# Kernel tuning notes

Hardware: AMD Instinct MI355X
Metric: run time of the kernel (lower is better)

The kernel has to match this reference:

```python
import jax, jax.numpy as jnp
import numpy as np

N_NODES = 40000
N_EDGES = 640000
IN_CH = 128
HID = 32
HEADS = 4
OUT_CH = 112
NEG_SLOPE = 0.2  # PyG GATConv default LeakyReLU slope


def _gat_conv(x, src, dst, W, a_src, a_dst, bias, heads, ch, concat):
    # x: [N, F_in], W: [F_in, heads*ch], a_src/a_dst: [heads, ch], bias: [heads*ch] or [ch]
    N = x.shape[0]
    h = (x @ W).reshape(N, heads, ch)                       # [N, H, C]
    al_src = jnp.sum(h * a_src, axis=-1)                    # [N, H]
    al_dst = jnp.sum(h * a_dst, axis=-1)                    # [N, H]
    e = jax.nn.leaky_relu(al_src[src] + al_dst[dst], NEG_SLOPE)  # [E, H]
    # numerically stable segment softmax over incoming edges of each dst node
    m = jax.ops.segment_max(e, dst, num_segments=N)
    m = jnp.where(jnp.isfinite(m), m, 0.0)
    ex = jnp.exp(e - m[dst])
    den = jax.ops.segment_sum(ex, dst, num_segments=N)
    alpha = ex / (den[dst] + 1e-16)                         # [E, H]
    out = jax.ops.segment_sum(h[src] * alpha[:, :, None], dst, num_segments=N)  # [N, H, C]
    out = out.reshape(N, heads * ch) if concat else out.mean(axis=1)
    return out + bias


def setup_inputs() -> dict:
    key = jax.random.key(0)
    ks = jax.random.split(key, 10)
    x = jax.random.normal(ks[0], (N_NODES, IN_CH), dtype=jnp.float32)
    edge_index = jax.random.randint(ks[1], (2, N_EDGES), 0, N_NODES, dtype=jnp.int64)
    s1 = 1.0 / np.sqrt(IN_CH)
    s2 = 1.0 / np.sqrt(HID * HEADS)
    s3 = 1.0 / np.sqrt(HID)
    return {
        "x": x,
        "edge_index": edge_index,
        "W1": jax.random.normal(ks[2], (IN_CH, HEADS * HID), dtype=jnp.float32) * s1,
        "a_src1": jax.random.normal(ks[3], (HEADS, HID), dtype=jnp.float32) * s3,
        "a_dst1": jax.random.normal(ks[4], (HEADS, HID), dtype=jnp.float32) * s3,
        "b1": jnp.zeros((HEADS * HID,), dtype=jnp.float32),
        "W2": jax.random.normal(ks[5], (HEADS * HID, HID), dtype=jnp.float32) * s2,
        "a_src2": jax.random.normal(ks[6], (1, HID), dtype=jnp.float32) * s3,
        "a_dst2": jax.random.normal(ks[7], (1, HID), dtype=jnp.float32) * s3,
        "b2": jnp.zeros((HID,), dtype=jnp.float32),
        "W_out": jax.random.normal(ks[8], (HID, OUT_CH), dtype=jnp.float32) * s3,
        "b_out": jnp.zeros((OUT_CH,), dtype=jnp.float32),
    }


def reference(x, edge_index, W1, a_src1, a_dst1, b1, W2, a_src2, a_dst2, b2, W_out, b_out):
    N = x.shape[0]
    # PyG GATConv adds self-loops by default
    loops = jnp.arange(N, dtype=edge_index.dtype)
    src = jnp.concatenate([edge_index[0], loops])
    dst = jnp.concatenate([edge_index[1], loops])
    h = _gat_conv(x, src, dst, W1, a_src1, a_dst1, b1, HEADS, HID, concat=True)
    h = jax.nn.elu(h)  # dropout is identity in eval mode
    h = _gat_conv(h, src, dst, W2, a_src2, a_dst2, b2, 1, HID, concat=True)
    h = jax.nn.elu(h)
    return h @ W_out + b_out
```

## Files before the change

### kernel.cpp

```cpp
#include <hip/hip_runtime.h>

#define N_NODES 40000
#define E_EDGES 640000
#define E_TOT   (E_EDGES + N_NODES)
#define SCAN_BLOCKS ((N_NODES + 255) / 256)
#define G1_BLOCKS 625
#define HIST_BLOCKS ((E_EDGES + 255) / 256)

typedef unsigned int uint;
typedef unsigned short ushort;
typedef __attribute__((ext_vector_type(8))) short short8v;
typedef __attribute__((ext_vector_type(4))) float f32x4;

__device__ __forceinline__ ushort f2bf(float f) {
    uint u = __float_as_uint(f);
    u += 0x7FFFu + ((u >> 16) & 1u);
    return (ushort)(u >> 16);
}
__device__ __forceinline__ uint pk_bf(float lo, float hi) {
    return (uint)f2bf(lo) | ((uint)f2bf(hi) << 16);
}
__device__ __forceinline__ float bf_lo(uint w) { return __uint_as_float(w << 16); }
__device__ __forceinline__ float bf_hi(uint w) { return __uint_as_float(w & 0xFFFF0000u); }
__device__ __forceinline__ float bf2f(ushort v) { return __uint_as_float((uint)v << 16); }

__global__ __launch_bounds__(256) void prep_kernel(
    const float* __restrict__ W1, int4* __restrict__ cnt4, ushort* __restrict__ Wf)
{
    if (blockIdx.x < 40) {
        const int i = blockIdx.x * 256 + threadIdx.x;
        if (i < 40064 / 4) cnt4[i] = make_int4(1, 1, 1, 1);
        return;
    }
    const int s = (blockIdx.x - 40) * 256 + threadIdx.x;
    if (s >= 2048) return;
    const int kk = s >> 9;
    const int rem = s & 511;
    const int ct = rem >> 6;
    const int l = rem & 63;
    const int k0 = kk * 32 + (l >> 4) * 8;
    const int col = ct * 16 + (l & 15);
    uint4 o;
    o.x = pk_bf(W1[(k0 + 0) * 128 + col], W1[(k0 + 1) * 128 + col]);
    o.y = pk_bf(W1[(k0 + 2) * 128 + col], W1[(k0 + 3) * 128 + col]);
    o.z = pk_bf(W1[(k0 + 4) * 128 + col], W1[(k0 + 5) * 128 + col]);
    o.w = pk_bf(W1[(k0 + 6) * 128 + col], W1[(k0 + 7) * 128 + col]);
    ((uint4*)Wf)[s] = o;
}

__global__ __launch_bounds__(256) void gemm1_hist_kernel(
    const float* __restrict__ x, const ushort* __restrict__ Wf,
    const float* __restrict__ a_src, const float* __restrict__ a_dst,
    ushort* __restrict__ h1b, float* __restrict__ asrc, float* __restrict__ adst,
    const int* __restrict__ eidx, int* __restrict__ cnt, int* __restrict__ rank)
{
    if (blockIdx.x >= G1_BLOCKS) {
        const int e = (blockIdx.x - G1_BLOCKS) * 256 + threadIdx.x;
        if (e < E_EDGES)
            rank[e] = atomicAdd(&cnt[eidx[E_EDGES + e]], 1);
        return;
    }

    const int wv = threadIdx.x >> 6;
    const int lane = threadIdx.x & 63;
    const int rowbase = blockIdx.x * 64 + wv * 16;
    const int arow = rowbase + (lane & 15);
    const int kof = (lane >> 4) * 8;

    f32x4 acc0 = {0.f,0.f,0.f,0.f}, acc1 = {0.f,0.f,0.f,0.f};
    f32x4 acc2 = {0.f,0.f,0.f,0.f}, acc3 = {0.f,0.f,0.f,0.f};
    f32x4 acc4 = {0.f,0.f,0.f,0.f}, acc5 = {0.f,0.f,0.f,0.f};
    f32x4 acc6 = {0.f,0.f,0.f,0.f}, acc7 = {0.f,0.f,0.f,0.f};

    const short8v* WfV = (const short8v*)Wf;
#pragma unroll
    for (int kk = 0; kk < 4; ++kk) {
        const float* ap = &x[(size_t)arow * 128 + kk * 32 + kof];
        const float4 a0 = *(const float4*)ap;
        const float4 a1 = *(const float4*)(ap + 4);
        short8v af;
        af[0] = (short)f2bf(a0.x); af[1] = (short)f2bf(a0.y);
        af[2] = (short)f2bf(a0.z); af[3] = (short)f2bf(a0.w);
        af[4] = (short)f2bf(a1.x); af[5] = (short)f2bf(a1.y);
        af[6] = (short)f2bf(a1.z); af[7] = (short)f2bf(a1.w);
        const int base = kk * 8 * 64 + lane;
        acc0 = __builtin_amdgcn_mfma_f32_16x16x32_bf16(af, WfV[base + 0 * 64], acc0, 0, 0, 0);
        acc1 = __builtin_amdgcn_mfma_f32_16x16x32_bf16(af, WfV[base + 1 * 64], acc1, 0, 0, 0);
        acc2 = __builtin_amdgcn_mfma_f32_16x16x32_bf16(af, WfV[base + 2 * 64], acc2, 0, 0, 0);
        acc3 = __builtin_amdgcn_mfma_f32_16x16x32_bf16(af, WfV[base + 3 * 64], acc3, 0, 0, 0);
        acc4 = __builtin_amdgcn_mfma_f32_16x16x32_bf16(af, WfV[base + 4 * 64], acc4, 0, 0, 0);
        acc5 = __builtin_amdgcn_mfma_f32_16x16x32_bf16(af, WfV[base + 5 * 64], acc5, 0, 0, 0);
        acc6 = __builtin_amdgcn_mfma_f32_16x16x32_bf16(af, WfV[base + 6 * 64], acc6, 0, 0, 0);
        acc7 = __builtin_amdgcn_mfma_f32_16x16x32_bf16(af, WfV[base + 7 * 64], acc7, 0, 0, 0);
    }

    const int cl = lane & 15;
    const int rg = lane >> 4;
    float csA[8], cdA[8];
#pragma unroll
    for (int ct = 0; ct < 8; ++ct) {
        csA[ct] = a_src[(ct >> 1) * 32 + (ct & 1) * 16 + cl];
        cdA[ct] = a_dst[(ct >> 1) * 32 + (ct & 1) * 16 + cl];
    }
    const f32x4 accv[8] = { acc0, acc1, acc2, acc3, acc4, acc5, acc6, acc7 };
#pragma unroll
    for (int r = 0; r < 4; ++r) {
        const int n = rowbase + rg * 4 + r;
        ushort* hrow = &h1b[(size_t)n * 128 + cl];
#pragma unroll
        for (int ct = 0; ct < 8; ++ct) hrow[ct * 16] = f2bf(accv[ct][r]);
#pragma unroll
        for (int h = 0; h < 4; ++h) {
            float ps = accv[2 * h][r] * csA[2 * h] + accv[2 * h + 1][r] * csA[2 * h + 1];
            float pd = accv[2 * h][r] * cdA[2 * h] + accv[2 * h + 1][r] * cdA[2 * h + 1];
            ps += __shfl_xor(ps, 1); ps += __shfl_xor(ps, 2);
            ps += __shfl_xor(ps, 4); ps += __shfl_xor(ps, 8);
            pd += __shfl_xor(pd, 1); pd += __shfl_xor(pd, 2);
            pd += __shfl_xor(pd, 4); pd += __shfl_xor(pd, 8);
            if (cl == 0) { asrc[n * 4 + h] = ps; adst[n * 4 + h] = pd; }
        }
    }
}

__global__ __launch_bounds__(256) void scanA_kernel(
    const int* __restrict__ cnt, int* __restrict__ rowptr, int* __restrict__ bsum)
{
    const int i = blockIdx.x * 256 + threadIdx.x;
    const int lane = threadIdx.x & 63;
    const int wave = threadIdx.x >> 6;
    const int v = (i < N_NODES) ? cnt[i] : 0;
    int incl = v;
#pragma unroll
    for (int off = 1; off < 64; off <<= 1) {
        int u = __shfl_up(incl, off);
        if (lane >= off) incl += u;
    }
    __shared__ int ws[4];
    if (lane == 63) ws[wave] = incl;
    __syncthreads();
    int woff = 0;
    if (wave > 0) woff += ws[0];
    if (wave > 1) woff += ws[1];
    if (wave > 2) woff += ws[2];
    if (i <= N_NODES) rowptr[i] = woff + incl - v;
    if (threadIdx.x == 255) bsum[blockIdx.x] = woff + incl;
}

__global__ __launch_bounds__(256) void scanB_kernel(int* __restrict__ bsum)
{
    const int t = threadIdx.x;
    const int lane = t & 63;
    const int wave = t >> 6;
    const int v = (t < SCAN_BLOCKS) ? bsum[t] : 0;
    int incl = v;
#pragma unroll
    for (int off = 1; off < 64; off <<= 1) {
        int u = __shfl_up(incl, off);
        if (lane >= off) incl += u;
    }
    __shared__ int ws[4];
    if (lane == 63) ws[wave] = incl;
    __syncthreads();
    int woff = 0;
    if (wave > 0) woff += ws[0];
    if (wave > 1) woff += ws[1];
    if (wave > 2) woff += ws[2];
    if (t < SCAN_BLOCKS) bsum[t] = woff + incl - v;
}

__global__ __launch_bounds__(256) void fill_kernel(
    const int* __restrict__ eidx, const int* __restrict__ rowptr,
    const int* __restrict__ bsum, const int* __restrict__ rank,
    int* __restrict__ esrc)
{
    const int e = blockIdx.x * 256 + threadIdx.x;
    if (e >= E_TOT) return;
    int s, d, r;
    if (e < E_EDGES) { s = eidx[e]; d = eidx[E_EDGES + e]; r = rank[e]; }
    else             { s = d = e - E_EDGES; r = 0; }
    esrc[rowptr[d] + bsum[d >> 8] + r] = s;
}

__global__ __launch_bounds__(256) void gather1_kernel(
    const int* __restrict__ rowptr, const int* __restrict__ bsum,
    const int* __restrict__ esrc, const float* __restrict__ asrc,
    const float* __restrict__ adst,
    const ushort* __restrict__ h1b, const float* __restrict__ b,
    float* __restrict__ agg)
{
    const int t = blockIdx.x * 256 + threadIdx.x;
    const int node = t >> 5;
    const int l32 = t & 31;
    const int head = l32 >> 3;
    const int cb = l32 * 4;
    const float ad = adst[node * 4 + head];
    const int beg = rowptr[node] + bsum[node >> 8];
    const int end = rowptr[node + 1] + bsum[(node + 1) >> 8];
    float acc0 = 0.f, acc1 = 0.f, acc2 = 0.f, acc3 = 0.f, den = 0.f;

    int i = beg;
    for (; i + 8 <= end; i += 8) {
        int s[8];
        float a[8];
        uint2 w[8];
#pragma unroll
        for (int j = 0; j < 8; ++j) s[j] = esrc[i + j];
#pragma unroll
        for (int j = 0; j < 8; ++j) a[j] = asrc[s[j] * 4 + head];
#pragma unroll
        for (int j = 0; j < 8; ++j)
            w[j] = *(const uint2*)&h1b[(size_t)s[j] * 128 + cb];
#pragma unroll
        for (int j = 0; j < 8; ++j) {
            float v = a[j] + ad; v = v > 0.f ? v : 0.2f * v;
            const float e = __expf(v);
            den += e;
            acc0 = fmaf(e, bf_lo(w[j].x), acc0);
            acc1 = fmaf(e, bf_hi(w[j].x), acc1);
            acc2 = fmaf(e, bf_lo(w[j].y), acc2);
            acc3 = fmaf(e, bf_hi(w[j].y), acc3);
        }
    }
    for (; i < end; ++i) {
        const int s = esrc[i];
        float av = asrc[s * 4 + head] + ad;
        av = av > 0.f ? av : 0.2f * av;
        const float ex = __expf(av);
        const uint2 w = *(const uint2*)&h1b[(size_t)s * 128 + cb];
        den += ex;
        acc0 = fmaf(ex, bf_lo(w.x), acc0);
        acc1 = fmaf(ex, bf_hi(w.x), acc1);
        acc2 = fmaf(ex, bf_lo(w.y), acc2);
        acc3 = fmaf(ex, bf_hi(w.y), acc3);
    }

    const float inv = 1.f / (den + 1e-16f);
    const float4 bv = *(const float4*)&b[cb];
    float o0 = acc0 * inv + bv.x;
    float o1 = acc1 * inv + bv.y;
    float o2 = acc2 * inv + bv.z;
    float o3 = acc3 * inv + bv.w;
    o0 = o0 > 0.f ? o0 : expm1f(o0);
    o1 = o1 > 0.f ? o1 : expm1f(o1);
    o2 = o2 > 0.f ? o2 : expm1f(o2);
    o3 = o3 > 0.f ? o3 : expm1f(o3);
    *(float4*)&agg[(size_t)node * 128 + cb] = make_float4(o0, o1, o2, o3);
}

__global__ __launch_bounds__(256) void gemm2_kernel(
    const float* __restrict__ hin, const float* __restrict__ W,
    const float* __restrict__ a_src, const float* __restrict__ a_dst,
    ushort* __restrict__ h2b, float* __restrict__ asrc, float* __restrict__ adst)
{
    __shared__ float Ws[128 * 32];
    {
        const float4* Wg = (const float4*)W;
        float4* Wl = (float4*)Ws;
        for (int i = threadIdx.x; i < 128 * 32 / 4; i += 256) Wl[i] = Wg[i];
    }
    __syncthreads();
    const int row0 = blockIdx.x * 64;
    const int tx = threadIdx.x & 7;
    const int ty = threadIdx.x >> 3;

    float acc[2][4];
#pragma unroll
    for (int r = 0; r < 2; ++r)
#pragma unroll
        for (int c = 0; c < 4; ++c) acc[r][c] = 0.f;

    for (int k0 = 0; k0 < 128; k0 += 4) {
        float xv[2][4];
#pragma unroll
        for (int r = 0; r < 2; ++r) {
            float4 t = *(const float4*)&hin[(size_t)(row0 + ty * 2 + r) * 128 + k0];
            xv[r][0] = t.x; xv[r][1] = t.y; xv[r][2] = t.z; xv[r][3] = t.w;
        }
#pragma unroll
        for (int kk = 0; kk < 4; ++kk) {
            float4 w = *(const float4*)&Ws[(k0 + kk) * 32 + tx * 4];
            float wreg[4] = { w.x, w.y, w.z, w.w };
#pragma unroll
            for (int r = 0; r < 2; ++r)
#pragma unroll
                for (int c = 0; c < 4; ++c)
                    acc[r][c] = fmaf(xv[r][kk], wreg[c], acc[r][c]);
        }
    }

    float as[4], ad[4];
#pragma unroll
    for (int c = 0; c < 4; ++c) {
        as[c] = a_src[tx * 4 + c];
        ad[c] = a_dst[tx * 4 + c];
    }
#pragma unroll
    for (int r = 0; r < 2; ++r) {
        const int n = row0 + ty * 2 + r;
        uint2 o;
        o.x = pk_bf(acc[r][0], acc[r][1]);
        o.y = pk_bf(acc[r][2], acc[r][3]);
        *(uint2*)&h2b[(size_t)n * 32 + tx * 4] = o;
        float ps = 0.f, pd = 0.f;
#pragma unroll
        for (int c = 0; c < 4; ++c) {
            ps = fmaf(acc[r][c], as[c], ps);
            pd = fmaf(acc[r][c], ad[c], pd);
        }
        ps += __shfl_xor(ps, 1); ps += __shfl_xor(ps, 2); ps += __shfl_xor(ps, 4);
        pd += __shfl_xor(pd, 1); pd += __shfl_xor(pd, 2); pd += __shfl_xor(pd, 4);
        if ((threadIdx.x & 7) == 0) { asrc[n] = ps; adst[n] = pd; }
    }
}

__global__ __launch_bounds__(256) void gather2_kernel(
    const int* __restrict__ rowptr, const int* __restrict__ bsum,
    const int* __restrict__ esrc,
    const float* __restrict__ asrc, const float* __restrict__ adst,
    const ushort* __restrict__ h2b, const float* __restrict__ b,
    float* __restrict__ agg)
{
    const int t = blockIdx.x * 256 + threadIdx.x;
    const int node = t >> 5;
    const int c = t & 31;
    if (node >= N_NODES) return;
    const float ad = adst[node];
    const int beg = rowptr[node] + bsum[node >> 8];
    const int end = rowptr[node + 1] + bsum[(node + 1) >> 8];
    float acc = 0.f, den = 0.f;

    int i = beg;
    for (; i + 8 <= end; i += 8) {
        int s[8];
        float a[8];
        ushort w[8];
#pragma unroll
        for (int j = 0; j < 8; ++j) s[j] = esrc[i + j];
#pragma unroll
        for (int j = 0; j < 8; ++j) a[j] = asrc[s[j]];
#pragma unroll
        for (int j = 0; j < 8; ++j) w[j] = h2b[(size_t)s[j] * 32 + c];
#pragma unroll
        for (int j = 0; j < 8; ++j) {
            float v = a[j] + ad; v = v > 0.f ? v : 0.2f * v;
            const float e = __expf(v);
            den += e;
            acc = fmaf(e, bf2f(w[j]), acc);
        }
    }
    for (; i < end; ++i) {
        const int s = esrc[i];
        float av = asrc[s] + ad;
        av = av > 0.f ? av : 0.2f * av;
        const float ex = __expf(av);
        den += ex;
        acc = fmaf(ex, bf2f(h2b[(size_t)s * 32 + c]), acc);
    }

    const float inv = 1.f / (den + 1e-16f);
    float o = acc * inv + b[c];
    o = o > 0.f ? o : expm1f(o);
    agg[(size_t)node * 32 + c] = o;
}

__global__ __launch_bounds__(256) void out_gemm_kernel(
    const float* __restrict__ h3, const float* __restrict__ W,
    const float* __restrict__ b, float* __restrict__ out)
{
    __shared__ float Ws[32 * 112];
    {
        const float4* Wg = (const float4*)W;
        float4* Wl = (float4*)Ws;
        for (int i = threadIdx.x; i < 32 * 112 / 4; i += 256) Wl[i] = Wg[i];
    }
    __syncthreads();
    const int row0 = blockIdx.x * 32;
    const int tc = threadIdx.x & 15;
    const int tr = threadIdx.x >> 4;

    float acc[2][7];
#pragma unroll
    for (int r = 0; r < 2; ++r)
#pragma unroll
        for (int c = 0; c < 7; ++c) acc[r][c] = 0.f;

    for (int k0 = 0; k0 < 32; k0 += 4) {
        float xv[2][4];
#pragma unroll
        for (int r = 0; r < 2; ++r) {
            float4 t = *(const float4*)&h3[(size_t)(row0 + tr * 2 + r) * 32 + k0];
            xv[r][0] = t.x; xv[r][1] = t.y; xv[r][2] = t.z; xv[r][3] = t.w;
        }
#pragma unroll
        for (int kk = 0; kk < 4; ++kk) {
            float wv[7];
#pragma unroll
            for (int c = 0; c < 7; ++c) wv[c] = Ws[(k0 + kk) * 112 + tc * 7 + c];
#pragma unroll
            for (int r = 0; r < 2; ++r)
#pragma unroll
                for (int c = 0; c < 7; ++c)
                    acc[r][c] = fmaf(xv[r][kk], wv[c], acc[r][c]);
        }
    }
#pragma unroll
    for (int r = 0; r < 2; ++r) {
        const int n = row0 + tr * 2 + r;
#pragma unroll
        for (int c = 0; c < 7; ++c)
            out[(size_t)n * 112 + tc * 7 + c] = acc[r][c] + b[tc * 7 + c];
    }
}

extern "C" void kernel_launch(void* const* d_in, const int* in_sizes, int n_in,
                              void* d_out, int out_size, void* d_ws, size_t ws_size,
                              hipStream_t stream) {
    const float* x      = (const float*)d_in[0];
    const int*   eidx   = (const int*)d_in[1];
    const float* W1     = (const float*)d_in[2];
    const float* a_src1 = (const float*)d_in[3];
    const float* a_dst1 = (const float*)d_in[4];
    const float* b1     = (const float*)d_in[5];
    const float* W2     = (const float*)d_in[6];
    const float* a_src2 = (const float*)d_in[7];
    const float* a_dst2 = (const float*)d_in[8];
    const float* b2     = (const float*)d_in[9];
    const float* W_out  = (const float*)d_in[10];
    const float* b_out  = (const float*)d_in[11];
    float* out = (float*)d_out;

    int* rowptr = (int*)d_ws;
    int* cnt    = rowptr + 40064;
    int* bsum   = cnt + 40064;
    int* rank   = bsum + 192;
    ushort* Wf  = (ushort*)(rank + 680000);
    int* esrc   = (int*)(Wf + 16384);
    ushort* h1b  = (ushort*)(esrc + 680000);
    float* asrc1 = (float*)(h1b + 5120000);
    float* adst1 = asrc1 + 160000;
    float* agg1  = adst1 + 160000;
    ushort* h2b  = (ushort*)h1b;
    float* asrc2 = (float*)(h2b + 1280000);
    float* adst2 = asrc2 + 40000;
    float* agg2  = adst2 + 40000;

    prep_kernel<<<48, 256, 0, stream>>>(W1, (int4*)cnt, Wf);

    gemm1_hist_kernel<<<G1_BLOCKS + HIST_BLOCKS, 256, 0, stream>>>(
        x, Wf, a_src1, a_dst1, h1b, asrc1, adst1, eidx, cnt, rank);

    scanA_kernel<<<SCAN_BLOCKS, 256, 0, stream>>>(cnt, rowptr, bsum);
    scanB_kernel<<<1, 256, 0, stream>>>(bsum);

    fill_kernel<<<(E_TOT + 255) / 256, 256, 0, stream>>>(
        eidx, rowptr, bsum, rank, esrc);

    gather1_kernel<<<5000, 256, 0, stream>>>(rowptr, bsum, esrc, asrc1, adst1,
                                             h1b, b1, agg1);

    gemm2_kernel<<<625, 256, 0, stream>>>(agg1, W2, a_src2, a_dst2, h2b, asrc2, adst2);
    gather2_kernel<<<5000, 256, 0, stream>>>(rowptr, bsum, esrc, asrc2, adst2,
                                             h2b, b2, agg2);

    out_gemm_kernel<<<1250, 256, 0, stream>>>(agg2, W_out, b_out, out);
}
```

Baseline: 131.4 us.

## Use bf16 MFMA for layer-2 and output GEMMs with bf16 intermediate activations

Both aggregation kernels now store their ELU outputs as bf16 instead of fp32, which halves intermediate traffic. The second-layer GEMM and the output GEMM are rewritten to use 16x16x32 bf16 MFMA instructions. Their weights are pre-packed into MFMA fragment layout in the prep kernel. This trades fp32 FMA loops over shared memory for matrix-core work and smaller reads, at the cost of extra bf16 rounding on the activations.

Result: faster. 119.1 us (-9.3%).

```diff
diff --git a/kernel.cpp b/kernel.cpp
--- a/kernel.cpp
+++ b/kernel.cpp
@@ -25,27 +25,62 @@
 __device__ __forceinline__ float bf2f(ushort v) { return __uint_as_float((uint)v << 16); }
 
 __global__ __launch_bounds__(256) void prep_kernel(
-    const float* __restrict__ W1, int4* __restrict__ cnt4, ushort* __restrict__ Wf)
+    const float* __restrict__ W1, const float* __restrict__ W2,
+    const float* __restrict__ W_out,
+    int4* __restrict__ cnt4, ushort* __restrict__ Wf,
+    ushort* __restrict__ Wf2, ushort* __restrict__ Wfo)
 {
     if (blockIdx.x < 40) {
         const int i = blockIdx.x * 256 + threadIdx.x;
         if (i < 40064 / 4) cnt4[i] = make_int4(1, 1, 1, 1);
         return;
     }
-    const int s = (blockIdx.x - 40) * 256 + threadIdx.x;
-    if (s >= 2048) return;
-    const int kk = s >> 9;
-    const int rem = s & 511;
-    const int ct = rem >> 6;
-    const int l = rem & 63;
-    const int k0 = kk * 32 + (l >> 4) * 8;
-    const int col = ct * 16 + (l & 15);
-    uint4 o;
-    o.x = pk_bf(W1[(k0 + 0) * 128 + col], W1[(k0 + 1) * 128 + col]);
-    o.y = pk_bf(W1[(k0 + 2) * 128 + col], W1[(k0 + 3) * 128 + col]);
-    o.z = pk_bf(W1[(k0 + 4) * 128 + col], W1[(k0 + 5) * 128 + col]);
-    o.w = pk_bf(W1[(k0 + 6) * 128 + col], W1[(k0 + 7) * 128 + col]);
-    ((uint4*)Wf)[s] = o;
+    if (blockIdx.x < 48) {
+        const int s = (blockIdx.x - 40) * 256 + threadIdx.x;
+        const int kk = s >> 9;
+        const int rem = s & 511;
+        const int ct = rem >> 6;
+        const int l = rem & 63;
+        const int k0 = kk * 32 + (l >> 4) * 8;
+        const int col = ct * 16 + (l & 15);
+        uint4 o;
+        o.x = pk_bf(W1[(k0 + 0) * 128 + col], W1[(k0 + 1) * 128 + col]);
+        o.y = pk_bf(W1[(k0 + 2) * 128 + col], W1[(k0 + 3) * 128 + col]);
+        o.z = pk_bf(W1[(k0 + 4) * 128 + col], W1[(k0 + 5) * 128 + col]);
+        o.w = pk_bf(W1[(k0 + 6) * 128 + col], W1[(k0 + 7) * 128 + col]);
+        ((uint4*)Wf)[s] = o;
+        return;
+    }
+    if (blockIdx.x < 50) {
+        const int s = (blockIdx.x - 48) * 256 + threadIdx.x;
+        const int kk = s >> 7;
+        const int rem = s & 127;
+        const int ct = rem >> 6;
+        const int l = rem & 63;
+        const int k0 = kk * 32 + (l >> 4) * 8;
+        const int col = ct * 16 + (l & 15);
+        uint4 o;
+        o.x = pk_bf(W2[(k0 + 0) * 32 + col], W2[(k0 + 1) * 32 + col]);
+        o.y = pk_bf(W2[(k0 + 2) * 32 + col], W2[(k0 + 3) * 32 + col]);
+        o.z = pk_bf(W2[(k0 + 4) * 32 + col], W2[(k0 + 5) * 32 + col]);
+        o.w = pk_bf(W2[(k0 + 6) * 32 + col], W2[(k0 + 7) * 32 + col]);
+        ((uint4*)Wf2)[s] = o;
+        return;
+    }
+    {
+        const int s = (blockIdx.x - 50) * 256 + threadIdx.x;
+        if (s >= 448) return;
+        const int ct = s >> 6;
+        const int l = s & 63;
+        const int k0 = (l >> 4) * 8;
+        const int col = ct * 16 + (l & 15);
+        uint4 o;
+        o.x = pk_bf(W_out[(k0 + 0) * 112 + col], W_out[(k0 + 1) * 112 + col]);
+        o.y = pk_bf(W_out[(k0 + 2) * 112 + col], W_out[(k0 + 3) * 112 + col]);
+        o.z = pk_bf(W_out[(k0 + 4) * 112 + col], W_out[(k0 + 5) * 112 + col]);
+        o.w = pk_bf(W_out[(k0 + 6) * 112 + col], W_out[(k0 + 7) * 112 + col]);
+        ((uint4*)Wfo)[s] = o;
+    }
 }
 
 __global__ __launch_bounds__(256) void gemm1_hist_kernel(
@@ -186,7 +221,7 @@
     const int* __restrict__ esrc, const float* __restrict__ asrc,
     const float* __restrict__ adst,
     const ushort* __restrict__ h1b, const float* __restrict__ b,
-    float* __restrict__ agg)
+    ushort* __restrict__ agg1b)
 {
     const int t = blockIdx.x * 256 + threadIdx.x;
     const int node = t >> 5;
@@ -244,72 +279,49 @@
     o1 = o1 > 0.f ? o1 : expm1f(o1);
     o2 = o2 > 0.f ? o2 : expm1f(o2);
     o3 = o3 > 0.f ? o3 : expm1f(o3);
-    *(float4*)&agg[(size_t)node * 128 + cb] = make_float4(o0, o1, o2, o3);
+    uint2 o;
+    o.x = pk_bf(o0, o1);
+    o.y = pk_bf(o2, o3);
+    *(uint2*)&agg1b[(size_t)node * 128 + cb] = o;
 }
 
 __global__ __launch_bounds__(256) void gemm2_kernel(
-    const float* __restrict__ hin, const float* __restrict__ W,
+    const ushort* __restrict__ agg1b, const ushort* __restrict__ Wf2,
     const float* __restrict__ a_src, const float* __restrict__ a_dst,
     ushort* __restrict__ h2b, float* __restrict__ asrc, float* __restrict__ adst)
 {
-    __shared__ float Ws[128 * 32];
-    {
-        const float4* Wg = (const float4*)W;
-        float4* Wl = (float4*)Ws;
-        for (int i = threadIdx.x; i < 128 * 32 / 4; i += 256) Wl[i] = Wg[i];
-    }
-    __syncthreads();
-    const int row0 = blockIdx.x * 64;
-    const int tx = threadIdx.x & 7;
-    const int ty = threadIdx.x >> 3;
-
-    float acc[2][4];
-#pragma unroll
-    for (int r = 0; r < 2; ++r)
-#pragma unroll
-        for (int c = 0; c < 4; ++c) acc[r][c] = 0.f;
-
-    for (int k0 = 0; k0 < 128; k0 += 4) {
-        float xv[2][4];
-#pragma unroll
-        for (int r = 0; r < 2; ++r) {
-            float4 t = *(const float4*)&hin[(size_t)(row0 + ty * 2 + r) * 128 + k0];
-            xv[r][0] = t.x; xv[r][1] = t.y; xv[r][2] = t.z; xv[r][3] = t.w;
-        }
-#pragma unroll
-        for (int kk = 0; kk < 4; ++kk) {
-            float4 w = *(const float4*)&Ws[(k0 + kk) * 32 + tx * 4];
-            float wreg[4] = { w.x, w.y, w.z, w.w };
-#pragma unroll
-            for (int r = 0; r < 2; ++r)
-#pragma unroll
-                for (int c = 0; c < 4; ++c)
-                    acc[r][c] = fmaf(xv[r][kk], wreg[c], acc[r][c]);
-        }
-    }
-
-    float as[4], ad[4];
-#pragma unroll
-    for (int c = 0; c < 4; ++c) {
-        as[c] = a_src[tx * 4 + c];
-        ad[c] = a_dst[tx * 4 + c];
-    }
-#pragma unroll
-    for (int r = 0; r < 2; ++r) {
-        const int n = row0 + ty * 2 + r;
-        uint2 o;
-        o.x = pk_bf(acc[r][0], acc[r][1]);
-        o.y = pk_bf(acc[r][2], acc[r][3]);
-        *(uint2*)&h2b[(size_t)n * 32 + tx * 4] = o;
-        float ps = 0.f, pd = 0.f;
-#pragma unroll
-        for (int c = 0; c < 4; ++c) {
-            ps = fmaf(acc[r][c], as[c], ps);
-            pd = fmaf(acc[r][c], ad[c], pd);
-        }
-        ps += __shfl_xor(ps, 1); ps += __shfl_xor(ps, 2); ps += __shfl_xor(ps, 4);
-        pd += __shfl_xor(pd, 1); pd += __shfl_xor(pd, 2); pd += __shfl_xor(pd, 4);
-        if ((threadIdx.x & 7) == 0) { asrc[n] = ps; adst[n] = pd; }
+    const int wv = threadIdx.x >> 6;
+    const int lane = threadIdx.x & 63;
+    const int rowbase = blockIdx.x * 64 + wv * 16;
+    const int arow = rowbase + (lane & 15);
+    const int kof = (lane >> 4) * 8;
+
+    f32x4 acc0 = {0.f,0.f,0.f,0.f}, acc1 = {0.f,0.f,0.f,0.f};
+    const short8v* Wf2V = (const short8v*)Wf2;
+#pragma unroll
+    for (int kk = 0; kk < 4; ++kk) {
+        const short8v af = *(const short8v*)&agg1b[(size_t)arow * 128 + kk * 32 + kof];
+        const int base = kk * 2 * 64 + lane;
+        acc0 = __builtin_amdgcn_mfma_f32_16x16x32_bf16(af, Wf2V[base], acc0, 0, 0, 0);
+        acc1 = __builtin_amdgcn_mfma_f32_16x16x32_bf16(af, Wf2V[base + 64], acc1, 0, 0, 0);
+    }
+
+    const int cl = lane & 15;
+    const int rg = lane >> 4;
+    const float cs0 = a_src[cl], cs1 = a_src[16 + cl];
+    const float cd0 = a_dst[cl], cd1 = a_dst[16 + cl];
+#pragma unroll
+    for (int r = 0; r < 4; ++r) {
+        const int n = rowbase + rg * 4 + r;
+        h2b[(size_t)n * 32 + cl]      = f2bf(acc0[r]);
+        h2b[(size_t)n * 32 + 16 + cl] = f2bf(acc1[r]);
+        float ps = acc0[r] * cs0 + acc1[r] * cs1;
+        float pd = acc0[r] * cd0 + acc1[r] * cd1;
+        ps += __shfl_xor(ps, 1); ps += __shfl_xor(ps, 2);
+        ps += __shfl_xor(ps, 4); ps += __shfl_xor(ps, 8);
+        pd += __shfl_xor(pd, 1); pd += __shfl_xor(pd, 2);
+        pd += __shfl_xor(pd, 4); pd += __shfl_xor(pd, 8);
+        if (cl == 0) { asrc[n] = ps; adst[n] = pd; }
     }
 }
 
@@ -318,7 +330,7 @@
     const int* __restrict__ esrc,
     const float* __restrict__ asrc, const float* __restrict__ adst,
     const ushort* __restrict__ h2b, const float* __restrict__ b,
-    float* __restrict__ agg)
+    ushort* __restrict__ agg2b)
 {
     const int t = blockIdx.x * 256 + threadIdx.x;
     const int node = t >> 5;
@@ -360,55 +372,39 @@
     const float inv = 1.f / (den + 1e-16f);
     float o = acc * inv + b[c];
     o = o > 0.f ? o : expm1f(o);
-    agg[(size_t)node * 32 + c] = o;
+    agg2b[(size_t)node * 32 + c] = f2bf(o);
 }
 
 __global__ __launch_bounds__(256) void out_gemm_kernel(
-    const float* __restrict__ h3, const float* __restrict__ W,
-    const float* __restrict__ b, float* __restrict__ out)
-{
-    __shared__ float Ws[32 * 112];
-    {
-        const float4* Wg = (const float4*)W;
-        float4* Wl = (float4*)Ws;
-        for (int i = threadIdx.x; i < 32 * 112 / 4; i += 256) Wl[i] = Wg[i];
-    }
-    __syncthreads();
-    const int row0 = blockIdx.x * 32;
-    const int tc = threadIdx.x & 15;
-    const int tr = threadIdx.x >> 4;
-
-    float acc[2][7];
-#pragma unroll
-    for (int r = 0; r < 2; ++r)
-#pragma unroll
-        for (int c = 0; c < 7; ++c) acc[r][c] = 0.f;
-
-    for (int k0 = 0; k0 < 32; k0 += 4) {
-        float xv[2][4];
-#pragma unroll
-        for (int r = 0; r < 2; ++r) {
-            float4 t = *(const float4*)&h3[(size_t)(row0 + tr * 2 + r) * 32 + k0];
-            xv[r][0] = t.x; xv[r][1] = t.y; xv[r][2] = t.z; xv[r][3] = t.w;
-        }
-#pragma unroll
-        for (int kk = 0; kk < 4; ++kk) {
-            float wv[7];
-#pragma unroll
-            for (int c = 0; c < 7; ++c) wv[c] = Ws[(k0 + kk) * 112 + tc * 7 + c];
-#pragma unroll
-            for (int r = 0; r < 2; ++r)
-#pragma unroll
-                for (int c = 0; c < 7; ++c)
-                    acc[r][c] = fmaf(xv[r][kk], wv[c], acc[r][c]);
-        }
-    }
-#pragma unroll
-    for (int r = 0; r < 2; ++r) {
-        const int n = row0 + tr * 2 + r;
-#pragma unroll
-        for (int c = 0; c < 7; ++c)
-            out[(size_t)n * 112 + tc * 7 + c] = acc[r][c] + b[tc * 7 + c];
+    const ushort* __restrict__ agg2b, const ushort* __restrict__ Wfo,
+    const float* __restrict__ b_out, float* __restrict__ out)
+{
+    const int wv = threadIdx.x >> 6;
+    const int lane = threadIdx.x & 63;
+    const int rowbase = blockIdx.x * 64 + wv * 16;
+    const int arow = rowbase + (lane & 15);
+    const int kof = (lane >> 4) * 8;
+
+    const short8v af = *(const short8v*)&agg2b[(size_t)arow * 32 + kof];
+    const short8v* WfoV = (const short8v*)Wfo;
+    f32x4 acc[7];
+#pragma unroll
+    for (int ct = 0; ct < 7; ++ct) {
+        f32x4 z = {0.f, 0.f, 0.f, 0.f};
+        acc[ct] = __builtin_amdgcn_mfma_f32_16x16x32_bf16(af, WfoV[ct * 64 + lane], z, 0, 0, 0);
+    }
+
+    const int cl = lane & 15;
+    const int rg = lane >> 4;
+    float bo[7];
+#pragma unroll
+    for (int ct = 0; ct < 7; ++ct) bo[ct] = b_out[ct * 16 + cl];
+#pragma unroll
+    for (int r = 0; r < 4; ++r) {
+        const int n = rowbase + rg * 4 + r;
+        float* orow = &out[(size_t)n * 112 + cl];
+#pragma unroll
+        for (int ct = 0; ct < 7; ++ct) orow[ct * 16] = acc[ct][r] + bo[ct];
     }
 }
 
@@ -434,17 +430,19 @@
     int* bsum   = cnt + 40064;
     int* rank   = bsum + 192;
     ushort* Wf  = (ushort*)(rank + 680000);
-    int* esrc   = (int*)(Wf + 16384);
+    ushort* Wf2 = Wf + 16384;
+    ushort* Wfo = Wf2 + 4096;
+    int* esrc   = (int*)(Wfo + 4096);
     ushort* h1b  = (ushort*)(esrc + 680000);
     float* asrc1 = (float*)(h1b + 5120000);
     float* adst1 = asrc1 + 160000;
-    float* agg1  = adst1 + 160000;
+    ushort* agg1b = (ushort*)(adst1 + 160000);
     ushort* h2b  = (ushort*)h1b;
     float* asrc2 = (float*)(h2b + 1280000);
     float* adst2 = asrc2 + 40000;
-    float* agg2  = adst2 + 40000;
-
-    prep_kernel<<<48, 256, 0, stream>>>(W1, (int4*)cnt, Wf);
+    ushort* agg2b = (ushort*)(adst2 + 40000);
+
+    prep_kernel<<<52, 256, 0, stream>>>(W1, W2, W_out, (int4*)cnt, Wf, Wf2, Wfo);
 
     gemm1_hist_kernel<<<G1_BLOCKS + HIST_BLOCKS, 256, 0, stream>>>(
         x, Wf, a_src1, a_dst1, h1b, asrc1, adst1, eidx, cnt, rank);
@@ -456,11 +454,12 @@
         eidx, rowptr, bsum, rank, esrc);
 
     gather1_kernel<<<5000, 256, 0, stream>>>(rowptr, bsum, esrc, asrc1, adst1,
-                                             h1b, b1, agg1);
-
-    gemm2_kernel<<<625, 256, 0, stream>>>(agg1, W2, a_src2, a_dst2, h2b, asrc2, adst2);
+                                             h1b, b1, agg1b);
+
+    gemm2_kernel<<<625, 256, 0, stream>>>(agg1b, Wf2, a_src2, a_dst2,
+                                          h2b, asrc2, adst2);
     gather2_kernel<<<5000, 256, 0, stream>>>(rowptr, bsum, esrc, asrc2, adst2,
-                                             h2b, b2, agg2);
-
-    out_gemm_kernel<<<1250, 256, 0, stream>>>(agg2, W_out, b_out, out);
-}
+                                             h2b, b2, agg2b);
+
+    out_gemm_kernel<<<625, 256, 0, stream>>>(agg2b, Wfo, b_out, out);
+}
```
